# Kernel tuning notes

Measured on AMD Instinct MI355X. Metric: run time of the kernel, lower is better.

The kernel has to match this reference:

```python
import jax, jax.numpy as jnp
import numpy as np

TRIANGLE_TABLE = np.array([
    [-1, -1, -1, -1, -1, -1], [1, 0, 2, -1, -1, -1], [4, 0, 3, -1, -1, -1], [1, 4, 2, 1, 3, 4],
    [3, 1, 5, -1, -1, -1], [2, 3, 0, 2, 5, 3], [1, 4, 0, 1, 5, 4], [4, 2, 5, -1, -1, -1],
    [4, 5, 2, -1, -1, -1], [4, 1, 0, 4, 5, 1], [3, 2, 0, 3, 5, 2], [1, 3, 5, -1, -1, -1],
    [4, 1, 2, 4, 3, 1], [3, 0, 4, -1, -1, -1], [2, 0, 1, -1, -1, -1], [-1, -1, -1, -1, -1, -1]], np.int32)
NUM_TRIANGLES_TABLE = np.array([0, 1, 1, 2, 1, 2, 2, 1, 1, 2, 2, 1, 2, 1, 1, 0], np.int32)
BASE_TET_EDGES = np.array([0, 1, 0, 2, 0, 3, 1, 2, 1, 3, 2, 3], np.int32)


def _make_tet_grid(R):
    # Regular grid in [0,1]^3, each cube split into 6 tets along the 0-7 diagonal.
    r1 = R + 1
    gi, gj, gk = np.meshgrid(np.arange(r1), np.arange(r1), np.arange(r1), indexing='ij')
    verts = (np.stack([gi, gj, gk], -1).reshape(-1, 3) / R).astype(np.float32)  # (Nv,3)
    ci, cj, ck = np.meshgrid(np.arange(R), np.arange(R), np.arange(R), indexing='ij')
    ci, cj, ck = ci.ravel(), cj.ravel(), ck.ravel()
    def vid(dx, dy, dz):
        return ((ci + dx) * r1 + (cj + dy)) * r1 + (ck + dz)
    corners = [vid((c >> 2) & 1, (c >> 1) & 1, c & 1) for c in range(8)]
    tet_corners = [(0, 1, 3, 7), (0, 3, 2, 7), (0, 2, 6, 7), (0, 6, 4, 7), (0, 4, 5, 7), (0, 5, 1, 7)]
    tets = np.stack([np.stack([corners[a] for a in t], -1) for t in tet_corners], 1).reshape(-1, 4)
    return verts, tets.astype(np.int32)


def setup_inputs() -> dict:
    R = 64
    verts, tets = _make_tet_grid(R)
    key = jax.random.key(0)
    k1, k2 = jax.random.split(key)
    level = jax.random.normal(k1, (verts.shape[0],), dtype=jnp.float32)
    deformation = jax.random.normal(k2, (verts.shape[0], 3), dtype=jnp.float32)
    return {
        'level': level,
        'deformation': deformation,
        'grid_vertices': jnp.asarray(verts),
        'tet_indices': jnp.asarray(tets),
        'resolution': R,
    }


def reference(level, deformation, grid_vertices, tet_indices, resolution):
    # normalize_grid_deformation: (range_hi - range_lo)/res * tanh(offsets), range = (0,1)
    pos = grid_vertices + jnp.tanh(deformation) / resolution  # (Nv,3)
    occ = level > 0                                           # (Nv,)
    occ_f = occ[tet_indices]                                  # (F,4)
    occ_sum = occ_f.sum(-1)
    valid = (occ_sum > 0) & (occ_sum < 4)
    vt = tet_indices[valid]                                   # (Fv,4)
    occ_valid = occ_f[valid]                                  # (Fv,4)
    # per-tet edges, each sorted (min,max) -> dedup
    edges = vt[:, jnp.asarray(BASE_TET_EDGES)].reshape(-1, 2)  # (6*Fv,2)
    edges = jnp.sort(edges, axis=1)
    unique_edges, idx_map = jnp.unique(edges, axis=0, return_inverse=True)
    idx_map = idx_map.reshape(-1)
    # edges that actually cross the isosurface (exactly one endpoint inside)
    mask_edges = occ[unique_edges].sum(-1) == 1               # (U,)
    mapping = jnp.where(mask_edges, jnp.cumsum(mask_edges.astype(jnp.int32)) - 1, -1)
    idx_map = mapping[idx_map].reshape(-1, 6)                 # (Fv,6)
    interp_v = unique_edges[mask_edges]                       # (M,2)
    # linear interpolation of crossing point along each edge
    ep = pos[interp_v]                                        # (M,2,3)
    es = level[interp_v] * jnp.array([1.0, -1.0], dtype=level.dtype)  # (M,2) = [sdf0, -sdf1]
    w = es[:, ::-1] / es.sum(1, keepdims=True)                # (M,2) = [-sdf1, sdf0]/(sdf0-sdf1)
    verts_out = (ep * w[:, :, None]).sum(1)                   # (M,3)
    # triangle table lookup
    v_id = jnp.array([1, 2, 4, 8], dtype=jnp.int32)
    tetindex = (occ_valid.astype(jnp.int32) * v_id).sum(-1)   # (Fv,)
    tri_tab = jnp.asarray(TRIANGLE_TABLE)
    num_tri = jnp.asarray(NUM_TRIANGLES_TABLE)[tetindex]
    m1 = num_tri == 1
    m2 = num_tri == 2
    f1 = jnp.take_along_axis(idx_map[m1], tri_tab[tetindex[m1]][:, :3], axis=1).reshape(-1, 3)
    f2 = jnp.take_along_axis(idx_map[m2], tri_tab[tetindex[m2]][:, :6], axis=1).reshape(-1, 3)
    faces = jnp.concatenate([f1, f2], axis=0)                 # (Nf,3)
    return verts_out, faces
```

## Files before the change

### kernel.cpp

```cpp
#include <hip/hip_runtime.h>
#include <math.h>


typedef unsigned long long ull;

#define ST_LD(p)    __hip_atomic_load((p), __ATOMIC_RELAXED, __HIP_MEMORY_SCOPE_AGENT)
#define ST_ST(p,v)  __hip_atomic_store((p), (v), __ATOMIC_RELAXED, __HIP_MEMORY_SCOPE_AGENT)

__device__ __forceinline__ float fast_tanh(float x) {
    float e = __expf(2.0f * x);
    return __fdividef(e - 1.0f, e + 1.0f);
}

__device__ __constant__ int c_tri_tab[16][6] = {
    {-1,-1,-1,-1,-1,-1},{1,0,2,-1,-1,-1},{4,0,3,-1,-1,-1},{1,4,2,1,3,4},
    {3,1,5,-1,-1,-1},{2,3,0,2,5,3},{1,4,0,1,5,4},{4,2,5,-1,-1,-1},
    {4,5,2,-1,-1,-1},{4,1,0,4,5,1},{3,2,0,3,5,2},{1,3,5,-1,-1,-1},
    {4,1,2,4,3,1},{3,0,4,-1,-1,-1},{2,0,1,-1,-1,-1},{-1,-1,-1,-1,-1,-1}};
__device__ __constant__ int c_num_tri[16] = {0,1,1,2,1,2,2,1,1,2,2,1,2,1,1,0};
__device__ __constant__ int c_tc[6][4] = {{0,1,3,7},{0,3,2,7},{0,2,6,7},{0,6,4,7},{0,4,5,7},{0,5,1,7}};
__device__ __constant__ int c_te[6][6] = {
    {(0<<3)|0,(0<<3)|2,(0<<3)|6,(1<<3)|1,(1<<3)|5,(3<<3)|3},
    {(0<<3)|2,(0<<3)|1,(0<<3)|6,(2<<3)|0,(3<<3)|3,(2<<3)|4},
    {(0<<3)|1,(0<<3)|5,(0<<3)|6,(2<<3)|3,(2<<3)|4,(6<<3)|0},
    {(0<<3)|5,(0<<3)|3,(0<<3)|6,(4<<3)|1,(6<<3)|0,(4<<3)|2},
    {(0<<3)|3,(0<<3)|4,(0<<3)|6,(4<<3)|0,(4<<3)|2,(5<<3)|1},
    {(0<<3)|4,(0<<3)|0,(0<<3)|6,(1<<3)|3,(5<<3)|1,(1<<3)|5}};

#define TAG      (1ull << 62)
#define PMASK    ((1ull << 60) - 1ull)
#define READY(s) (((s) >> 62) == 1ull)

__global__ void k_vert(const float* __restrict__ level, const float* __restrict__ deform,
                       int NV, int r1, float invR,
                       ull* __restrict__ stateA,
                       unsigned* __restrict__ rankWord, ull* __restrict__ cubeInfo,
                       int* __restrict__ totals, ull* __restrict__ dtab,
                       float* __restrict__ out) {
    int b = blockIdx.x;
    int v = b * 256 + threadIdx.x;
    int R = r1 - 1, rsq = r1 * r1;
    bool valid = v < NV;
    float la = valid ? level[v] : 0.f;
    bool occv = valid && (la > 0.f);

    int x = 0, y = 0, z = 0, flags = 0, n1 = 0, n2 = 0, cidx = 0, ob = 0;
    bool interior = false;
    float lb[7];
    if (valid) {
        x = v / rsq; int rem = v - x * rsq; y = rem / r1; z = rem - y * r1;
        bool bx = x < R, by = y < R, bz = z < R;
        interior = bx && by && bz;
        bool inb[7] = {bz, by, by && bz, bx, bx && bz, bx && by, interior};
        int deltas[7] = {1, r1, r1 + 1, rsq, rsq + 1, rsq + r1, rsq + r1 + 1};
        ob = occv ? 1 : 0;
        for (int j = 0; j < 7; j++) {
            float l = inb[j] ? level[v + deltas[j]] : 0.f;
            lb[j] = l;
            bool o = inb[j] && (l > 0.f);
            ob |= (o ? 1 : 0) << (j + 1);
            if (inb[j] && (o != occv)) flags |= 1 << j;
        }
        if (interior) {
            cidx = ((x * R) + y) * R + z;
            for (int k = 0; k < 6; k++) {
                int ti = ((ob >> c_tc[k][0]) & 1) | (((ob >> c_tc[k][1]) & 1) << 1)
                       | (((ob >> c_tc[k][2]) & 1) << 2) | (((ob >> c_tc[k][3]) & 1) << 3);
                int n = c_num_tri[ti];
                n1 += (n == 1); n2 += (n == 2);
            }
        }
    }
    int cnt = __popc(flags);
    int pk = n1 | (n2 << 16);
    int lane = threadIdx.x & 63, wv = threadIdx.x >> 6;
    int inclE = cnt, inclT = pk;
    for (int o = 1; o < 64; o <<= 1) {
        int tE = __shfl_up(inclE, o);
        int tT = __shfl_up(inclT, o);
        if (lane >= o) { inclE += tE; inclT += tT; }
    }
    __shared__ int wE[4], wT[4];
    __shared__ ull sPart[4];
    if (lane == 63) { wE[wv] = inclE; wT[wv] = inclT; }
    __syncthreads();

    if (threadIdx.x == 0) {
        int eb = wE[0] + wE[1] + wE[2] + wE[3];
        int tb = wT[0] + wT[1] + wT[2] + wT[3];
        ST_ST(&stateA[b], TAG | ((ull)eb << 40) | ((ull)(tb & 0xffff) << 20) | (ull)(tb >> 16));
    }
    ull psum = 0;
    for (int t = 0;; t++) {
        int base = 64 * (4 * t + wv);
        if (base >= b) break;
        int i = b - 1 - (base + lane);
        ull s = 0;
        if (i >= 0) {
            do { s = ST_LD(&stateA[i]); } while (!READY(s));
            s &= PMASK;
        }
        psum += s;
    }
    for (int o = 1; o < 64; o <<= 1) psum += __shfl_xor(psum, o);
    if (lane == 0) sPart[wv] = psum;
    __syncthreads();

    ull ex = sPart[0] + sPart[1] + sPart[2] + sPart[3];
    int exclE = (int)((ex >> 40) & 0xFFFFF);
    int excl1 = (int)((ex >> 20) & 0xFFFFF);
    int excl2 = (int)(ex & 0xFFFFF);
    int eb2 = wE[0] + wE[1] + wE[2] + wE[3];
    if (threadIdx.x == 0 && b == (int)gridDim.x - 1) {
        int tb = wT[0] + wT[1] + wT[2] + wT[3];
        ull inc = ex + (((ull)eb2 << 40) | ((ull)(tb & 0xffff) << 20) | (ull)(tb >> 16));
        totals[0] = (int)((inc >> 40) & 0xFFFFF);
        totals[1] = (int)((inc >> 20) & 0xFFFFF);
        totals[2] = (int)(inc & 0xFFFFF);
    }
    int woffE = 0, woffT = 0;
    for (int w2 = 0; w2 < wv; w2++) { woffE += wE[w2]; woffT += wT[w2]; }
    int rank0 = exclE + woffE + inclE - cnt;
    int tExcl = woffT + inclT - pk;
    if (interior)
        cubeInfo[cidx] = (ull)(unsigned)ob
                       | ((ull)(unsigned)(excl1 + (tExcl & 0xffff)) << 8)
                       | ((ull)(unsigned)(excl2 + (tExcl >> 16)) << 28);
    if (valid)
        rankWord[v] = (unsigned)rank0 | ((unsigned)flags << 21);

    __shared__ float ldsV[5376];
    if (flags) {
        int deltas[7] = {1, r1, r1 + 1, rsq, rsq + 1, rsq + r1, rsq + r1 + 1};
        const int dxs[7] = {0, 0, 0, 1, 1, 1, 1};
        const int dys[7] = {0, 1, 1, 0, 0, 1, 1};
        const int dzs[7] = {1, 0, 1, 0, 1, 0, 1};
        float pax = x * invR + fast_tanh(deform[3 * v])     * invR;
        float pay = y * invR + fast_tanh(deform[3 * v + 1]) * invR;
        float paz = z * invR + fast_tanh(deform[3 * v + 2]) * invR;
        int r = rank0 - exclE;
        for (int j = 0; j < 7; j++) {
            if (!((flags >> j) & 1)) continue;
            int bb = v + deltas[j];
            float lbv = lb[j];
            float inv = __fdividef(1.0f, la - lbv);
            float w0 = -lbv * inv;
            float w1f = la * inv;
            float pbx = (x + dxs[j]) * invR + fast_tanh(deform[3 * bb])     * invR;
            float pby = (y + dys[j]) * invR + fast_tanh(deform[3 * bb + 1]) * invR;
            float pbz = (z + dzs[j]) * invR + fast_tanh(deform[3 * bb + 2]) * invR;
            ldsV[3 * r]     = pax * w0 + pbx * w1f;
            ldsV[3 * r + 1] = pay * w0 + pby * w1f;
            ldsV[3 * r + 2] = paz * w0 + pbz * w1f;
            r++;
        }
    }
    __syncthreads();
    int tot = 3 * eb2;
    float* dstV = out + 3 * (size_t)exclE;
    for (int i = threadIdx.x; i < tot; i += 256) dstV[i] = ldsV[i];

    if (b < 8) {
        int idx = b * 256 + threadIdx.x;
        int obt = idx >> 3, k = idx & 7;
        ull w = 0;
        if (k < 6) {
            int ti = ((obt >> c_tc[k][0]) & 1) | (((obt >> c_tc[k][1]) & 1) << 1)
                   | (((obt >> c_tc[k][2]) & 1) << 2) | (((obt >> c_tc[k][3]) & 1) << 3);
            int nt = c_num_tri[ti];
            int pre1 = 0, pre2 = 0;
            for (int kk = 0; kk < k; kk++) {
                int tik = ((obt >> c_tc[kk][0]) & 1) | (((obt >> c_tc[kk][1]) & 1) << 1)
                        | (((obt >> c_tc[kk][2]) & 1) << 2) | (((obt >> c_tc[kk][3]) & 1) << 3);
                int m = c_num_tri[tik];
                pre1 += (m == 1); pre2 += (m == 2);
            }
            w = (ull)nt | ((ull)pre1 << 2) | ((ull)pre2 << 5);
            for (int e = 0; e < 6; e++) {
                int le = c_tri_tab[ti][e];
                int ce = (le >= 0) ? c_te[k][le] : 0;
                w |= (ull)ce << (8 + 6 * e);
            }
        }
        dtab[idx] = w;
    }
}

__device__ __forceinline__ unsigned sel8(int c, unsigned r0, unsigned r1_, unsigned r2,
                                         unsigned r3, unsigned r4, unsigned r5,
                                         unsigned r6, unsigned r7) {
    unsigned a01 = (c & 1) ? r1_ : r0;
    unsigned a23 = (c & 1) ? r3 : r2;
    unsigned a45 = (c & 1) ? r5 : r4;
    unsigned a67 = (c & 1) ? r7 : r6;
    unsigned lo = (c & 2) ? a23 : a01;
    unsigned hi = (c & 2) ? a67 : a45;
    return (c & 4) ? hi : lo;
}

__global__ void k_face(int r1, int NC,
                       const ull* __restrict__ cubeInfo,
                       const unsigned* __restrict__ rankWord,
                       const int* __restrict__ totals,
                       const ull* __restrict__ dtab,
                       float* __restrict__ out) {
    int tid = threadIdx.x;
    int c = blockIdx.x * 256 + tid;
    bool act = c < NC;
    int rsq = r1 * r1, R = r1 - 1, rr = R * R;

    ull info = 0;
    ull w0 = 0, w1 = 0, w2 = 0, w3 = 0, w4 = 0, w5 = 0;
    unsigned rw0=0,rw1=0,rw2=0,rw3=0,rw4=0,rw5=0,rw6=0,rw7=0;
    if (act) {
        info = cubeInfo[c];
        int ob = (int)info & 255;
        const ull* dp = dtab + (ob << 3);
        ulonglong2 p0 = *reinterpret_cast<const ulonglong2*>(dp);
        ulonglong2 p1 = *reinterpret_cast<const ulonglong2*>(dp + 2);
        ulonglong2 p2 = *reinterpret_cast<const ulonglong2*>(dp + 4);
        w0 = p0.x; w1 = p0.y; w2 = p1.x; w3 = p1.y; w4 = p2.x; w5 = p2.y;
        int cx = c / rr; int rem = c - cx * rr; int cy = rem / R; int cz = rem - cy * R;
        int v = (cx * r1 + cy) * r1 + cz;
        rw0 = rankWord[v];             rw1 = rankWord[v + 1];
        rw2 = rankWord[v + r1];        rw3 = rankWord[v + r1 + 1];
        rw4 = rankWord[v + rsq];       rw5 = rankWord[v + rsq + 1];
        rw6 = rankWord[v + rsq + r1];  rw7 = rankWord[v + rsq + r1 + 1];
    }
    unsigned r1c = (unsigned)((info >> 8) & 0xFFFFF);
    unsigned r2c = (unsigned)((info >> 28) & 0xFFFFF);
    int nt5 = (int)w5 & 3;
    int n1c = (((int)w5 >> 2) & 7) + (nt5 == 1);
    int n2c = (((int)w5 >> 5) & 7) + (nt5 == 2);

    __shared__ unsigned sB1, sB2, sE1, sE2;
    __shared__ float ldsF[9216];
    int lastT = NC - 1 - blockIdx.x * 256; if (lastT > 255) lastT = 255;
    if (tid == 0)     { sB1 = r1c; sB2 = r2c; }
    if (tid == lastT) { sE1 = r1c + (unsigned)n1c; sE2 = r2c + (unsigned)n2c; }
    __syncthreads();

    int n1b = (int)(sE1 - sB1), n2b = (int)(sE2 - sB2);
    float* Lr1 = ldsF;
    float* Lr2 = ldsF + 3 * n1b;

    #define ERANK(ce_)                                                          \
        ({ int ce = (ce_);                                                      \
           unsigned rw = sel8(ce >> 3, rw0,rw1,rw2,rw3,rw4,rw5,rw6,rw7);        \
           (float)((int)(rw & 0x1FFFFF) + __popc((rw >> 21) & ((1u << (ce & 7)) - 1u))); })

    if (act) {
        int local1 = (int)(r1c - sB1);
        int local2 = (int)(r2c - sB2);
        #define DO_TET(wk) do {                                                 \
            int nt = (int)(wk) & 3;                                             \
            if (nt) {                                                           \
                ull we = (wk) >> 8;                                             \
                if (nt == 1) {                                                  \
                    int s = local1 + (((int)(wk) >> 2) & 7);                    \
                    float* d = &Lr1[3 * s];                                     \
                    d[0] = ERANK((int)(we) & 63);                               \
                    d[1] = ERANK((int)(we >> 6) & 63);                          \
                    d[2] = ERANK((int)(we >> 12) & 63);                         \
                } else {                                                        \
                    int s = local2 + (((int)(wk) >> 5) & 7);                    \
                    float* d = &Lr2[6 * s];                                     \
                    d[0] = ERANK((int)(we) & 63);                               \
                    d[1] = ERANK((int)(we >> 6) & 63);                          \
                    d[2] = ERANK((int)(we >> 12) & 63);                         \
                    d[3] = ERANK((int)(we >> 18) & 63);                         \
                    d[4] = ERANK((int)(we >> 24) & 63);                         \
                    d[5] = ERANK((int)(we >> 30) & 63);                         \
                }                                                               \
            }                                                                   \
        } while (0)
        DO_TET(w0); DO_TET(w1); DO_TET(w2); DO_TET(w3); DO_TET(w4); DO_TET(w5);
        #undef DO_TET
    }
    #undef ERANK
    __syncthreads();

    int M = totals[0], N1 = totals[1];
    float* faces = out + 3 * (size_t)M;
    float* d1 = faces + 3 * (size_t)sB1;
    for (int i = tid; i < 3 * n1b; i += 256) d1[i] = ldsF[i];
    float* d2 = faces + 3 * (size_t)N1 + 6 * (size_t)sB2;
    const float* s2 = ldsF + 3 * n1b;
    for (int i = tid; i < 6 * n2b; i += 256) d2[i] = s2[i];
}

extern "C" void kernel_launch(void* const* d_in, const int* in_sizes, int n_in,
                              void* d_out, int out_size, void* d_ws, size_t ws_size,
                              hipStream_t stream) {
    const float* level  = (const float*)d_in[0];
    const float* deform = (const float*)d_in[1];
    int NV = in_sizes[0];
    int r1 = 1;
    while ((long long)r1 * r1 * r1 < (long long)NV) r1++;
    int R = r1 - 1;
    float invR = 1.0f / (float)R;

    int nb = (NV + 255) / 256;
    int NC = R * R * R;
    int nbC = (NC + 255) / 256;

    char* w = (char*)d_ws;
    unsigned* rankWord = (unsigned*)w;
    w += (((size_t)NV * sizeof(unsigned)) + 255) & ~(size_t)255;
    ull* cubeInfo = (ull*)w;
    w += (((size_t)NC * 8) + 255) & ~(size_t)255;
    ull* stateA = (ull*)w;
    w += (((size_t)nb * 8) + 255) & ~(size_t)255;
    int* totals = (int*)w;
    w += 256;
    ull* dtab = (ull*)w;

    float* out = (float*)d_out;

    k_vert<<<nb, 256, 0, stream>>>(level, deform, NV, r1, invR, stateA,
                                   rankWord, cubeInfo, totals, dtab, out);
    k_face<<<nbC, 256, 0, stream>>>(r1, NC, cubeInfo, rankWord, totals, dtab, out);
}
```

Measured before the change: 113.5 us.

## Overlap vertex interpolation with lookback; precompute face table at compile time

Moves the edge-crossing vertex interpolation ahead of the decoupled-lookback spin. Each block's heavy compute can then hide the wait on its predecessors' prefix state. The per-ob triangle descriptor table is now built by a constexpr function into constant memory instead of being written by the first blocks of k_vert, which removes that dependency and workspace traffic. It also swaps the integer divisions for precomputed multiply-shift reciprocals, derives the triangle count from popcount, and unrolls the small loops. The risks are higher register pressure from the reordering and divergent per-thread reads of the constant table.

Result: faster. 111.1 us (median of 2 runs) (-2.1%).

```diff
diff --git a/kernel.cpp b/kernel.cpp
--- a/kernel.cpp
+++ b/kernel.cpp
@@ -12,14 +12,18 @@
     return __fdividef(e - 1.0f, e + 1.0f);
 }
 
-__device__ __constant__ int c_tri_tab[16][6] = {
+__device__ __forceinline__ int divq(unsigned v, ull M) {
+    return (int)(((ull)v * M) >> 46);
+}
+
+constexpr int TT[16][6] = {
     {-1,-1,-1,-1,-1,-1},{1,0,2,-1,-1,-1},{4,0,3,-1,-1,-1},{1,4,2,1,3,4},
     {3,1,5,-1,-1,-1},{2,3,0,2,5,3},{1,4,0,1,5,4},{4,2,5,-1,-1,-1},
     {4,5,2,-1,-1,-1},{4,1,0,4,5,1},{3,2,0,3,5,2},{1,3,5,-1,-1,-1},
     {4,1,2,4,3,1},{3,0,4,-1,-1,-1},{2,0,1,-1,-1,-1},{-1,-1,-1,-1,-1,-1}};
-__device__ __constant__ int c_num_tri[16] = {0,1,1,2,1,2,2,1,1,2,2,1,2,1,1,0};
-__device__ __constant__ int c_tc[6][4] = {{0,1,3,7},{0,3,2,7},{0,2,6,7},{0,6,4,7},{0,4,5,7},{0,5,1,7}};
-__device__ __constant__ int c_te[6][6] = {
+constexpr int NTRI[16] = {0,1,1,2,1,2,2,1,1,2,2,1,2,1,1,0};
+constexpr int TC[6][4] = {{0,1,3,7},{0,3,2,7},{0,2,6,7},{0,6,4,7},{0,4,5,7},{0,5,1,7}};
+constexpr int TE[6][6] = {
     {(0<<3)|0,(0<<3)|2,(0<<3)|6,(1<<3)|1,(1<<3)|5,(3<<3)|3},
     {(0<<3)|2,(0<<3)|1,(0<<3)|6,(2<<3)|0,(3<<3)|3,(2<<3)|4},
     {(0<<3)|1,(0<<3)|5,(0<<3)|6,(2<<3)|3,(2<<3)|4,(6<<3)|0},
@@ -27,16 +31,45 @@
     {(0<<3)|3,(0<<3)|4,(0<<3)|6,(4<<3)|0,(4<<3)|2,(5<<3)|1},
     {(0<<3)|4,(0<<3)|0,(0<<3)|6,(1<<3)|3,(5<<3)|1,(1<<3)|5}};
 
+struct DTabT { ull w[2048]; };
+constexpr DTabT make_dtab() {
+    DTabT t{};
+    for (int ob = 0; ob < 256; ob++) {
+        for (int k = 0; k < 8; k++) {
+            ull w = 0;
+            if (k < 6) {
+                int ti = ((ob >> TC[k][0]) & 1) | (((ob >> TC[k][1]) & 1) << 1)
+                       | (((ob >> TC[k][2]) & 1) << 2) | (((ob >> TC[k][3]) & 1) << 3);
+                int nt = NTRI[ti];
+                int pre1 = 0, pre2 = 0;
+                for (int kk = 0; kk < k; kk++) {
+                    int tik = ((ob >> TC[kk][0]) & 1) | (((ob >> TC[kk][1]) & 1) << 1)
+                            | (((ob >> TC[kk][2]) & 1) << 2) | (((ob >> TC[kk][3]) & 1) << 3);
+                    pre1 += (NTRI[tik] == 1); pre2 += (NTRI[tik] == 2);
+                }
+                w = (ull)nt | ((ull)pre1 << 2) | ((ull)pre2 << 5);
+                for (int e = 0; e < 6; e++) {
+                    int le = TT[ti][e];
+                    int ce = (le >= 0) ? TE[k][le] : 0;
+                    w |= (ull)ce << (8 + 6 * e);
+                }
+            }
+            t.w[ob * 8 + k] = w;
+        }
+    }
+    return t;
+}
+__device__ __constant__ DTabT c_dtab = make_dtab();
+
 #define TAG      (1ull << 62)
 #define PMASK    ((1ull << 60) - 1ull)
 #define READY(s) (((s) >> 62) == 1ull)
 
 __global__ void k_vert(const float* __restrict__ level, const float* __restrict__ deform,
-                       int NV, int r1, float invR,
+                       int NV, int r1, float invR, ull Mrsq, ull Mr1,
                        ull* __restrict__ stateA,
                        unsigned* __restrict__ rankWord, ull* __restrict__ cubeInfo,
-                       int* __restrict__ totals, ull* __restrict__ dtab,
-                       float* __restrict__ out) {
+                       int* __restrict__ totals, float* __restrict__ out) {
     int b = blockIdx.x;
     int v = b * 256 + threadIdx.x;
     int R = r1 - 1, rsq = r1 * r1;
@@ -48,12 +81,14 @@
     bool interior = false;
     float lb[7];
     if (valid) {
-        x = v / rsq; int rem = v - x * rsq; y = rem / r1; z = rem - y * r1;
+        x = divq((unsigned)v, Mrsq); int rem = v - x * rsq;
+        y = divq((unsigned)rem, Mr1); z = rem - y * r1;
         bool bx = x < R, by = y < R, bz = z < R;
         interior = bx && by && bz;
         bool inb[7] = {bz, by, by && bz, bx, bx && bz, bx && by, interior};
         int deltas[7] = {1, r1, r1 + 1, rsq, rsq + 1, rsq + r1, rsq + r1 + 1};
         ob = occv ? 1 : 0;
+        #pragma unroll
         for (int j = 0; j < 7; j++) {
             float l = inb[j] ? level[v + deltas[j]] : 0.f;
             lb[j] = l;
@@ -63,11 +98,13 @@
         }
         if (interior) {
             cidx = ((x * R) + y) * R + z;
+            #pragma unroll
             for (int k = 0; k < 6; k++) {
-                int ti = ((ob >> c_tc[k][0]) & 1) | (((ob >> c_tc[k][1]) & 1) << 1)
-                       | (((ob >> c_tc[k][2]) & 1) << 2) | (((ob >> c_tc[k][3]) & 1) << 3);
-                int n = c_num_tri[ti];
-                n1 += (n == 1); n2 += (n == 2);
+                int ti = ((ob >> TC[k][0]) & 1) | (((ob >> TC[k][1]) & 1) << 1)
+                       | (((ob >> TC[k][2]) & 1) << 2) | (((ob >> TC[k][3]) & 1) << 3);
+                int p = __popc(ti);
+                n1 += (p == 1) || (p == 3);
+                n2 += (p == 2);
             }
         }
     }
@@ -75,6 +112,7 @@
     int pk = n1 | (n2 << 16);
     int lane = threadIdx.x & 63, wv = threadIdx.x >> 6;
     int inclE = cnt, inclT = pk;
+    #pragma unroll
     for (int o = 1; o < 64; o <<= 1) {
         int tE = __shfl_up(inclE, o);
         int tT = __shfl_up(inclT, o);
@@ -90,6 +128,40 @@
         int tb = wT[0] + wT[1] + wT[2] + wT[3];
         ST_ST(&stateA[b], TAG | ((ull)eb << 40) | ((ull)(tb & 0xffff) << 20) | (ull)(tb >> 16));
     }
+    int woffE = 0, woffT = 0;
+    for (int w2 = 0; w2 < wv; w2++) { woffE += wE[w2]; woffT += wT[w2]; }
+    int localRank = woffE + inclE - cnt;
+    int tExcl = woffT + inclT - pk;
+
+    __shared__ float ldsV[5376];
+    if (flags) {
+        int deltas[7] = {1, r1, r1 + 1, rsq, rsq + 1, rsq + r1, rsq + r1 + 1};
+        const int dxs[7] = {0, 0, 0, 1, 1, 1, 1};
+        const int dys[7] = {0, 1, 1, 0, 0, 1, 1};
+        const int dzs[7] = {1, 0, 1, 0, 1, 0, 1};
+        float pax = x * invR + fast_tanh(deform[3 * v])     * invR;
+        float pay = y * invR + fast_tanh(deform[3 * v + 1]) * invR;
+        float paz = z * invR + fast_tanh(deform[3 * v + 2]) * invR;
+        int r = localRank;
+        #pragma unroll
+        for (int j = 0; j < 7; j++) {
+            if ((flags >> j) & 1) {
+                int bb = v + deltas[j];
+                float lbv = lb[j];
+                float inv = __fdividef(1.0f, la - lbv);
+                float w0 = -lbv * inv;
+                float w1f = la * inv;
+                float pbx = (x + dxs[j]) * invR + fast_tanh(deform[3 * bb])     * invR;
+                float pby = (y + dys[j]) * invR + fast_tanh(deform[3 * bb + 1]) * invR;
+                float pbz = (z + dzs[j]) * invR + fast_tanh(deform[3 * bb + 2]) * invR;
+                ldsV[3 * r]     = pax * w0 + pbx * w1f;
+                ldsV[3 * r + 1] = pay * w0 + pby * w1f;
+                ldsV[3 * r + 2] = paz * w0 + pbz * w1f;
+                r++;
+            }
+        }
+    }
+
     ull psum = 0;
     for (int t = 0;; t++) {
         int base = 64 * (4 * t + wv);
@@ -102,6 +174,7 @@
         }
         psum += s;
     }
+    #pragma unroll
     for (int o = 1; o < 64; o <<= 1) psum += __shfl_xor(psum, o);
     if (lane == 0) sPart[wv] = psum;
     __syncthreads();
@@ -118,72 +191,16 @@
         totals[1] = (int)((inc >> 20) & 0xFFFFF);
         totals[2] = (int)(inc & 0xFFFFF);
     }
-    int woffE = 0, woffT = 0;
-    for (int w2 = 0; w2 < wv; w2++) { woffE += wE[w2]; woffT += wT[w2]; }
-    int rank0 = exclE + woffE + inclE - cnt;
-    int tExcl = woffT + inclT - pk;
     if (interior)
         cubeInfo[cidx] = (ull)(unsigned)ob
                        | ((ull)(unsigned)(excl1 + (tExcl & 0xffff)) << 8)
                        | ((ull)(unsigned)(excl2 + (tExcl >> 16)) << 28);
     if (valid)
-        rankWord[v] = (unsigned)rank0 | ((unsigned)flags << 21);
-
-    __shared__ float ldsV[5376];
-    if (flags) {
-        int deltas[7] = {1, r1, r1 + 1, rsq, rsq + 1, rsq + r1, rsq + r1 + 1};
-        const int dxs[7] = {0, 0, 0, 1, 1, 1, 1};
-        const int dys[7] = {0, 1, 1, 0, 0, 1, 1};
-        const int dzs[7] = {1, 0, 1, 0, 1, 0, 1};
-        float pax = x * invR + fast_tanh(deform[3 * v])     * invR;
-        float pay = y * invR + fast_tanh(deform[3 * v + 1]) * invR;
-        float paz = z * invR + fast_tanh(deform[3 * v + 2]) * invR;
-        int r = rank0 - exclE;
-        for (int j = 0; j < 7; j++) {
-            if (!((flags >> j) & 1)) continue;
-            int bb = v + deltas[j];
-            float lbv = lb[j];
-            float inv = __fdividef(1.0f, la - lbv);
-            float w0 = -lbv * inv;
-            float w1f = la * inv;
-            float pbx = (x + dxs[j]) * invR + fast_tanh(deform[3 * bb])     * invR;
-            float pby = (y + dys[j]) * invR + fast_tanh(deform[3 * bb + 1]) * invR;
-            float pbz = (z + dzs[j]) * invR + fast_tanh(deform[3 * bb + 2]) * invR;
-            ldsV[3 * r]     = pax * w0 + pbx * w1f;
-            ldsV[3 * r + 1] = pay * w0 + pby * w1f;
-            ldsV[3 * r + 2] = paz * w0 + pbz * w1f;
-            r++;
-        }
-    }
-    __syncthreads();
+        rankWord[v] = (unsigned)(exclE + localRank) | ((unsigned)flags << 21);
+
     int tot = 3 * eb2;
     float* dstV = out + 3 * (size_t)exclE;
     for (int i = threadIdx.x; i < tot; i += 256) dstV[i] = ldsV[i];
-
-    if (b < 8) {
-        int idx = b * 256 + threadIdx.x;
-        int obt = idx >> 3, k = idx & 7;
-        ull w = 0;
-        if (k < 6) {
-            int ti = ((obt >> c_tc[k][0]) & 1) | (((obt >> c_tc[k][1]) & 1) << 1)
-                   | (((obt >> c_tc[k][2]) & 1) << 2) | (((obt >> c_tc[k][3]) & 1) << 3);
-            int nt = c_num_tri[ti];
-            int pre1 = 0, pre2 = 0;
-            for (int kk = 0; kk < k; kk++) {
-                int tik = ((obt >> c_tc[kk][0]) & 1) | (((obt >> c_tc[kk][1]) & 1) << 1)
-                        | (((obt >> c_tc[kk][2]) & 1) << 2) | (((obt >> c_tc[kk][3]) & 1) << 3);
-                int m = c_num_tri[tik];
-                pre1 += (m == 1); pre2 += (m == 2);
-            }
-            w = (ull)nt | ((ull)pre1 << 2) | ((ull)pre2 << 5);
-            for (int e = 0; e < 6; e++) {
-                int le = c_tri_tab[ti][e];
-                int ce = (le >= 0) ? c_te[k][le] : 0;
-                w |= (ull)ce << (8 + 6 * e);
-            }
-        }
-        dtab[idx] = w;
-    }
 }
 
 __device__ __forceinline__ unsigned sel8(int c, unsigned r0, unsigned r1_, unsigned r2,
@@ -198,11 +215,10 @@
     return (c & 4) ? hi : lo;
 }
 
-__global__ void k_face(int r1, int NC,
+__global__ void k_face(int r1, int NC, ull Mrr, ull MR,
                        const ull* __restrict__ cubeInfo,
                        const unsigned* __restrict__ rankWord,
                        const int* __restrict__ totals,
-                       const ull* __restrict__ dtab,
                        float* __restrict__ out) {
     int tid = threadIdx.x;
     int c = blockIdx.x * 256 + tid;
@@ -215,12 +231,13 @@
     if (act) {
         info = cubeInfo[c];
         int ob = (int)info & 255;
-        const ull* dp = dtab + (ob << 3);
+        const ull* dp = &c_dtab.w[ob << 3];
         ulonglong2 p0 = *reinterpret_cast<const ulonglong2*>(dp);
         ulonglong2 p1 = *reinterpret_cast<const ulonglong2*>(dp + 2);
         ulonglong2 p2 = *reinterpret_cast<const ulonglong2*>(dp + 4);
         w0 = p0.x; w1 = p0.y; w2 = p1.x; w3 = p1.y; w4 = p2.x; w5 = p2.y;
-        int cx = c / rr; int rem = c - cx * rr; int cy = rem / R; int cz = rem - cy * R;
+        int cx = divq((unsigned)c, Mrr); int rem = c - cx * rr;
+        int cy = divq((unsigned)rem, MR); int cz = rem - cy * R;
         int v = (cx * r1 + cy) * r1 + cz;
         rw0 = rankWord[v];             rw1 = rankWord[v + 1];
         rw2 = rankWord[v + r1];        rw3 = rankWord[v + r1 + 1];
@@ -299,6 +316,12 @@
     while ((long long)r1 * r1 * r1 < (long long)NV) r1++;
     int R = r1 - 1;
     float invR = 1.0f / (float)R;
+    int rsq = r1 * r1, rr = R * R;
+
+    ull Mrsq = ((1ull << 46) + (ull)rsq - 1) / (ull)rsq;
+    ull Mr1  = ((1ull << 46) + (ull)r1  - 1) / (ull)r1;
+    ull Mrr  = ((1ull << 46) + (ull)rr  - 1) / (ull)rr;
+    ull MR   = ((1ull << 46) + (ull)R   - 1) / (ull)R;
 
     int nb = (NV + 255) / 256;
     int NC = R * R * R;
@@ -312,12 +335,10 @@
     ull* stateA = (ull*)w;
     w += (((size_t)nb * 8) + 255) & ~(size_t)255;
     int* totals = (int*)w;
-    w += 256;
-    ull* dtab = (ull*)w;
 
     float* out = (float*)d_out;
 
-    k_vert<<<nb, 256, 0, stream>>>(level, deform, NV, r1, invR, stateA,
-                                   rankWord, cubeInfo, totals, dtab, out);
-    k_face<<<nbC, 256, 0, stream>>>(r1, NC, cubeInfo, rankWord, totals, dtab, out);
-}
+    k_vert<<<nb, 256, 0, stream>>>(level, deform, NV, r1, invR, Mrsq, Mr1,
+                                   stateA, rankWord, cubeInfo, totals, out);
+    k_face<<<nbC, 256, 0, stream>>>(r1, NC, Mrr, MR, cubeInfo, rankWord, totals, out);
+}
```
